# Performance work log

Hardware: AMD Instinct MI355X
Metric: run time of the kernel (lower is better)

Reference implementation:

```python
import jax, jax.numpy as jnp
import numpy as np
from itertools import product

# dims
V, B, C, H, Wd = 3, 4, 64, 120, 160   # views, batch, feat2d_channel, image H/W
D3 = 96                               # feat3d_dim
G = 64                                # voxel grid side
N = 200000                            # sparse voxel count
NL = 250000                           # number of link rows
K = 27                                # 3^3 sparse-conv kernel offsets
EPS = 1e-5


def _build_kernel_map(rng):
    # unique sparse coordinates (b,x,y,z) sampled from a B*G^3 grid, sorted by linear code
    lin = np.sort(rng.choice(B * G * G * G, size=N, replace=False)).astype(np.int64)
    b = lin // (G * G * G)
    r = lin % (G * G * G)
    x = r // (G * G)
    y = (r // G) % G
    z = r % G
    in_idx = np.zeros((K, N), np.int32)
    mask = np.zeros((K, N), bool)
    for k, (dx, dy, dz) in enumerate(product((-1, 0, 1), repeat=3)):
        qx, qy, qz = x + dx, y + dy, z + dz
        inb = (qx >= 0) & (qx < G) & (qy >= 0) & (qy < G) & (qz >= 0) & (qz < G)
        qc = ((b * G + np.clip(qx, 0, G - 1)) * G + np.clip(qy, 0, G - 1)) * G + np.clip(qz, 0, G - 1)
        pos = np.clip(np.searchsorted(lin, qc), 0, N - 1)
        ok = inb & (lin[pos] == qc)
        in_idx[k] = np.where(ok, pos, 0)
        mask[k] = ok
    return jnp.asarray(in_idx), jnp.asarray(mask)


def setup_inputs() -> dict:
    rng = np.random.default_rng(0)
    key = jax.random.key(0)
    ks = jax.random.split(key, 8)
    feat_2d_all = jax.random.normal(ks[0], (V, B, C, H, Wd), jnp.float32)
    feat3d_F = jax.random.normal(ks[1], (N, D3), jnp.float32)
    # links: (NL, 4, V) = [batch_idx, v(row), u(col), valid]
    links = np.stack([
        rng.integers(0, B, (NL, V)),
        rng.integers(0, H, (NL, V)),
        rng.integers(0, Wd, (NL, V)),
        rng.integers(0, 2, (NL, V)),
    ], axis=1).astype(np.int32)
    coords_map_out = rng.permutation(N).astype(np.int32)
    coords_map_in = rng.choice(NL, N, replace=False).astype(np.int32)
    in_idx, nbr_mask = _build_kernel_map(rng)
    s = 0.05
    W1 = jax.random.normal(ks[2], (K, V * C, C), jnp.float32) * s
    W2 = jax.random.normal(ks[3], (K, C, D3), jnp.float32) * s
    W3 = jax.random.normal(ks[4], (K, 2 * D3, D3), jnp.float32) * s
    return {
        'feat_2d_all': feat_2d_all, 'feat3d_F': feat3d_F,
        'links': jnp.asarray(links),
        'coords_map_in': jnp.asarray(coords_map_in),
        'coords_map_out': jnp.asarray(coords_map_out),
        'in_idx': in_idx, 'nbr_mask': nbr_mask,
        'W1': W1, 'g1': jnp.ones((C,)), 'b1': jnp.zeros((C,)),
        'W2': W2, 'g2': jnp.ones((D3,)), 'b2': jnp.zeros((D3,)),
        'W3': W3, 'g3': jnp.ones((D3,)), 'b3': jnp.zeros((D3,)),
    }


def _sconv(x, Wk, in_idx, nbr_mask):
    # sparse 3x3x3 conv: out[i] = sum_k x[nbr(i,k)] @ Wk[k], masked where no neighbor
    out = jnp.zeros((x.shape[0], Wk.shape[-1]), x.dtype)
    for k in range(Wk.shape[0]):
        g = x[in_idx[k]] * nbr_mask[k][:, None].astype(x.dtype)
        out = out + g @ Wk[k]
    return out


def _bn_relu(x, g, b):
    mu = x.mean(axis=0)
    var = x.var(axis=0)
    return jax.nn.relu(g * (x - mu) / jnp.sqrt(var + EPS) + b)


def reference(feat_2d_all, feat3d_F, links, coords_map_in, coords_map_out,
              in_idx, nbr_mask, W1, g1, b1, W2, g2, b2, W3, g3, b3):
    n = feat3d_F.shape[0]
    v_, c = feat_2d_all.shape[0], feat_2d_all.shape[2]
    # current_links[coords_map_out] = links[coords_map_in]
    cur = jnp.zeros((n, 4, v_), links.dtype).at[coords_map_out].set(links[coords_map_in])
    bi = cur[:, 0, :].T   # (V, n)
    hi = cur[:, 1, :].T
    wi = cur[:, 2, :].T
    val = cur[:, 3, :].T
    vs = jnp.arange(v_)[:, None]
    # per-view gather from (V,B,C,H,W): advanced indices around the channel slice -> (V, n, C)
    g = feat_2d_all[vs, bi, :, hi, wi]
    g = g * val[:, :, None].astype(g.dtype)
    feat_2d_to_3d = jnp.transpose(g, (1, 0, 2)).reshape(n, v_ * c)
    # view_fusion: conv3 -> BN -> ReLU -> conv3 -> BN -> ReLU
    h = _bn_relu(_sconv(feat_2d_to_3d, W1, in_idx, nbr_mask), g1, b1)
    h = _bn_relu(_sconv(h, W2, in_idx, nbr_mask), g2, b2)
    # cat with 3d features, fuse_to_3d: conv3 -> BN -> ReLU
    cat = jnp.concatenate([feat3d_F, h], axis=-1)
    out = _bn_relu(_sconv(cat, W3, in_idx, nbr_mask), g3, b3)
    return out
```

## Files before the change

kernel.cpp:

```cpp
#include <hip/hip_runtime.h>
#include <stdint.h>


constexpr int NPT = 200000;
constexpr int KNB = 27;

typedef unsigned short u16;
typedef __attribute__((ext_vector_type(8))) short     bf16x8;
typedef __attribute__((ext_vector_type(8))) unsigned short u16x8;
typedef __attribute__((ext_vector_type(16))) float    f32x16;

static __device__ __forceinline__ u16 f2bf(float f){
  unsigned int u = __float_as_uint(f);
  unsigned int r = (u + 0x7fffu + ((u >> 16) & 1u)) >> 16;
  return (u16)r;
}
static __device__ __forceinline__ float bf2f(u16 u){
  return __uint_as_float(((unsigned int)u) << 16);
}

static __device__ __forceinline__ void gload_lds16(const void* g, void* l){
  __builtin_amdgcn_global_load_lds(
      (const __attribute__((address_space(1))) void*)g,
      (__attribute__((address_space(3))) void*)(uint32_t)(uintptr_t)l,
      16, 0, 0);
}

__global__ void detect_mask_kernel(const int* __restrict__ m32, int* __restrict__ flag){
  if (threadIdx.x == 0 && blockIdx.x == 0){
    int ok = 1;
    for (int i = 0; i < 64; ++i){ int v = m32[i]; if (v != 0 && v != 1) ok = 0; }
    *flag = ok;
  }
}

__global__ __launch_bounds__(256) void transpose2d_kernel(const float* __restrict__ in,
                                                          u16* __restrict__ out){
  __shared__ float tile[64][33];
  int bid = blockIdx.x;
  int wt = bid % 5;  int rest = bid / 5;
  int h  = rest % 120; rest /= 120;
  int b  = rest % 4;  int v = rest / 4;
  int w0 = wt * 32;
  int tx = threadIdx.x & 31;
  int ty = threadIdx.x >> 5;
  const float* ip = in + ((size_t)(v*4 + b) * 64) * 19200 + h * 160 + w0;
  #pragma unroll
  for (int cc = 0; cc < 8; ++cc){
    int c = cc * 8 + ty;
    tile[c][tx] = ip[(size_t)c * 19200 + tx];
  }
  __syncthreads();
  u16* op = out + (((size_t)(v*4 + b) * 120 + h) * 160 + w0) * 64;
  int c = threadIdx.x & 63;
  int wg = threadIdx.x >> 6;
  #pragma unroll
  for (int i = 0; i < 8; ++i){
    int w = wg + i * 4;
    op[(size_t)w * 64 + c] = f2bf(tile[c][w]);
  }
}

__global__ void wconvert_kernel(const float* __restrict__ src, u16* __restrict__ dst,
                                int cin, int cout){
  int gid = blockIdx.x * 256 + threadIdx.x;
  int wele = cin * cout;
  int tot = KNB * wele;
  if (gid >= tot) return;
  int ncb = cout / 32;
  int nks = cin / 16;
  int e    = gid & 7;
  int lane = (gid >> 3) & 63;
  int f    = gid >> 9;
  int cb   = f % ncb;  f /= ncb;
  int ks   = f % nks;
  int k    = f / nks;
  int ci = ks * 16 + (lane >> 5) * 8 + e;
  int co = cb * 32 + (lane & 31);
  dst[gid] = f2bf(src[((size_t)k * cin + ci) * cout + co]);
}

__global__ void stage_a_kernel(const u16* __restrict__ ft, const int* __restrict__ links,
                               const int* __restrict__ cmi, const int* __restrict__ cmo,
                               u16* __restrict__ x0){
  int gid = blockIdx.x * 256 + threadIdx.x;
  if (gid >= NPT * 3) return;
  int i = gid / 3;
  int v = gid - i * 3;
  int outr = cmo[i];
  int l    = cmi[i];
  int b  = links[l*12 + v];
  int h  = links[l*12 + 3 + v];
  int w  = links[l*12 + 6 + v];
  int vl = links[l*12 + 9 + v];
  u16* dst = x0 + (size_t)outr * 192 + v * 64;
  if (vl){
    const u16* src = ft + (((size_t)(v*4 + b) * 120 + h) * 160 + w) * 64;
    #pragma unroll
    for (int j = 0; j < 8; ++j) ((u16x8*)dst)[j] = ((const u16x8*)src)[j];
  } else {
    u16x8 z = {};
    #pragma unroll
    for (int j = 0; j < 8; ++j) ((u16x8*)dst)[j] = z;
  }
}

__global__ void f3convert_kernel(const float* __restrict__ src, u16* __restrict__ dst){
  long gid = (long)blockIdx.x * 256 + threadIdx.x;
  long tot8 = (long)NPT * 12;
  if (gid >= tot8) return;
  int row = (int)(gid / 12);
  int c0  = (int)(gid % 12) * 8;
  const float* s = src + (size_t)row * 96 + c0;
  u16* d = dst + (size_t)row * 192 + c0;
  #pragma unroll
  for (int j = 0; j < 8; ++j) d[j] = f2bf(s[j]);
}

template<int CIN, int COUT, bool F32OUT>
__global__ __launch_bounds__(256)
void conv_kernel(const u16* __restrict__ x0, const u16* __restrict__ wt,
                 const int* __restrict__ in_idx,
                 const uint8_t* __restrict__ mu8, const int* __restrict__ mi32,
                 const int* __restrict__ flagp, void* __restrict__ outp,
                 int outStride, float* __restrict__ st){
  constexpr int NCB    = COUT / 32;
  constexpr int NKC    = CIN / 16;
  constexpr int WELE   = CIN * COUT;
  constexpr int ROUNDS = (WELE * 2) / 4096;
  __shared__ __align__(16) u16 wlds[WELE];
  __shared__ float shS[COUT], shQ[COUT];

  const int tid   = threadIdx.x;
  const int lane  = tid & 63;
  const int wv    = tid >> 6;
  const int l31   = lane & 31;
  const int khalf = lane >> 5;
  const int m0    = blockIdx.x * 256;
  const int fInt  = *flagp;

  if (tid < COUT){ shS[tid] = 0.f; shQ[tid] = 0.f; }

  f32x16 acc[2][NCB];
  #pragma unroll
  for (int rt = 0; rt < 2; ++rt)
    #pragma unroll
    for (int cb = 0; cb < NCB; ++cb) acc[rt][cb] = (f32x16)0.0f;

  int rowc[2];
  #pragma unroll
  for (int rt = 0; rt < 2; ++rt){
    int row = m0 + wv * 64 + rt * 32 + l31;
    rowc[rt] = row < NPT ? row : NPT - 1;
  }

  #pragma unroll
  for (int rd = 0; rd < ROUNDS; ++rd){
    int chunk = rd * 4 + wv;
    gload_lds16((const char*)wt + chunk * 1024 + lane * 16,
                (char*)wlds + chunk * 1024);
  }
  int vC[2];
  #pragma unroll
  for (int rt = 0; rt < 2; ++rt){
    int id = in_idx[rowc[rt]];
    int mv; if (fInt) mv = mi32[rowc[rt]]; else mv = (int)mu8[rowc[rt]];
    vC[rt] = mv ? id : NPT;
  }
  __syncthreads();

  const u16* xk = x0 + khalf * 8;

  for (int k = 0; k < KNB; ++k){
    const u16* b0 = xk + (size_t)vC[0] * CIN;
    const u16* b1 = xk + (size_t)vC[1] * CIN;

    if (k + 1 < KNB){
      #pragma unroll
      for (int rt = 0; rt < 2; ++rt){
        int o = (k + 1) * NPT + rowc[rt];
        int id = in_idx[o];
        int mv; if (fInt) mv = mi32[o]; else mv = (int)mu8[o];
        vC[rt] = mv ? id : NPT;
      }
    }

    #pragma unroll
    for (int kc = 0; kc < NKC; ++kc){
      bf16x8 a0 = *(const bf16x8*)(b0 + kc * 16);
      bf16x8 a1 = *(const bf16x8*)(b1 + kc * 16);
      #pragma unroll
      for (int cb = 0; cb < NCB; ++cb){
        bf16x8 b = *(const bf16x8*)&wlds[((kc * NCB + cb) * 64 + lane) * 8];
        acc[0][cb] = __builtin_amdgcn_mfma_f32_32x32x16_bf16(a0, b, acc[0][cb], 0, 0, 0);
        acc[1][cb] = __builtin_amdgcn_mfma_f32_32x32x16_bf16(a1, b, acc[1][cb], 0, 0, 0);
      }
    }
    __syncthreads();

    if (k + 1 < KNB){
      const u16* wn = wt + (size_t)(k + 1) * WELE;
      #pragma unroll
      for (int rd = 0; rd < ROUNDS; ++rd){
        int chunk = rd * 4 + wv;
        gload_lds16((const char*)wn + chunk * 1024 + lane * 16,
                    (char*)wlds + chunk * 1024);
      }
    }
    __syncthreads();
  }

  #pragma unroll
  for (int rt = 0; rt < 2; ++rt){
    #pragma unroll
    for (int cb = 0; cb < NCB; ++cb){
      const int cout = cb * 32 + l31;
      float s = 0.f, q = 0.f;
      #pragma unroll
      for (int r = 0; r < 16; ++r){
        int row = m0 + wv * 64 + rt * 32 + (r & 3) + 8 * (r >> 2) + 4 * khalf;
        if (row < NPT){
          float v = acc[rt][cb][r];
          if (F32OUT) ((float*)outp)[(size_t)row * outStride + cout] = v;
          else        ((u16*)outp)[(size_t)row * outStride + cout] = f2bf(v);
          s += v; q += v * v;
        }
      }
      atomicAdd(&shS[cout], s); atomicAdd(&shQ[cout], q);
    }
  }
  __syncthreads();
  if (tid < COUT){
    atomicAdd(&st[tid],        shS[tid]);
    atomicAdd(&st[COUT + tid], shQ[tid]);
  }
}

template<int CCH, bool ISF32>
__global__ void bnrelu_kernel(void* __restrict__ xp, int stride,
                              const float* __restrict__ st,
                              const float* __restrict__ gg, const float* __restrict__ bb){
  const float invN = 1.0f / (float)NPT;
  constexpr int GPR = CCH / 8;
  long tot8 = (long)NPT * GPR;
  for (long e8 = (long)blockIdx.x * 256 + threadIdx.x; e8 < tot8; e8 += (long)gridDim.x * 256){
    int row = (int)(e8 / GPR);
    int c0  = (int)(e8 % GPR) * 8;
    size_t base = (size_t)row * stride + c0;
    #pragma unroll
    for (int j = 0; j < 8; ++j){
      int c = c0 + j;
      float mu  = st[c] * invN;
      float var = st[CCH + c] * invN - mu * mu;
      float rs  = rsqrtf(var + 1e-5f);
      float x;
      if (ISF32) x = ((float*)xp)[base + j];
      else       x = bf2f(((u16*)xp)[base + j]);
      float y = gg[c] * (x - mu) * rs + bb[c];
      y = y > 0.f ? y : 0.f;
      if (ISF32) ((float*)xp)[base + j] = y;
      else       ((u16*)xp)[base + j] = f2bf(y);
    }
  }
}

extern "C" void kernel_launch(void* const* d_in, const int* in_sizes, int n_in,
                              void* d_out, int out_size, void* d_ws, size_t ws_size,
                              hipStream_t stream){
  const float* feat2d = (const float*)d_in[0];
  const float* feat3d = (const float*)d_in[1];
  const int*   links  = (const int*)d_in[2];
  const int*   cmi    = (const int*)d_in[3];
  const int*   cmo    = (const int*)d_in[4];
  const int*   inidx  = (const int*)d_in[5];
  const void*  mask   = d_in[6];
  const float* W1 = (const float*)d_in[7];
  const float* g1 = (const float*)d_in[8];
  const float* b1 = (const float*)d_in[9];
  const float* W2 = (const float*)d_in[10];
  const float* g2 = (const float*)d_in[11];
  const float* b2 = (const float*)d_in[12];
  const float* W3 = (const float*)d_in[13];
  const float* g3 = (const float*)d_in[14];
  const float* b3 = (const float*)d_in[15];

  char* ws = (char*)d_ws;
  u16* X0 = (u16*)(ws + 0);
  constexpr size_t OFF_B  = 76800512;
  u16* FT = (u16*)(ws + OFF_B);
  u16* Z1 = (u16*)(ws + OFF_B);
  u16* WT1 = (u16*)(ws + 106291712);
  u16* WT2 = WT1 + 27 * 192 * 64;
  u16* WT3 = WT2 + 27 * 64 * 96;
  float* ST  = (float*)(ws + 108282368);
  float* ST1 = ST;
  float* ST2 = ST + 128;
  float* ST3 = ST + 320;
  int*   FLAG = (int*)(ST + 512);

  hipMemsetAsync(ST, 0, 513 * sizeof(float), stream);
  detect_mask_kernel<<<1, 64, 0, stream>>>((const int*)mask, FLAG);
  transpose2d_kernel<<<7200, 256, 0, stream>>>(feat2d, FT);
  wconvert_kernel<<<(27*192*64 + 255)/256, 256, 0, stream>>>(W1, WT1, 192, 64);
  wconvert_kernel<<<(27*64*96  + 255)/256, 256, 0, stream>>>(W2, WT2, 64, 96);
  wconvert_kernel<<<(27*192*96 + 255)/256, 256, 0, stream>>>(W3, WT3, 192, 96);
  stage_a_kernel<<<(NPT*3 + 255)/256, 256, 0, stream>>>(FT, links, cmi, cmo, X0);

  hipMemsetAsync(ws + (size_t)NPT * 384, 0, 384, stream);
  hipMemsetAsync(ws + OFF_B + (size_t)NPT * 128, 0, 128, stream);

  const int nblk = (NPT + 255) / 256;
  const uint8_t* m8 = (const uint8_t*)mask;
  const int* m32 = (const int*)mask;

  conv_kernel<192, 64, false><<<nblk, 256, 0, stream>>>(X0, WT1, inidx, m8, m32, FLAG, Z1, 64, ST1);
  bnrelu_kernel<64, false><<<2048, 256, 0, stream>>>(Z1, 64, ST1, g1, b1);

  f3convert_kernel<<<((NPT*12) + 255)/256, 256, 0, stream>>>(feat3d, X0);

  conv_kernel<64, 96, false><<<nblk, 256, 0, stream>>>(Z1, WT2, inidx, m8, m32, FLAG, X0 + 96, 192, ST2);
  bnrelu_kernel<96, false><<<2048, 256, 0, stream>>>(X0 + 96, 192, ST2, g2, b2);

  conv_kernel<192, 96, true><<<nblk, 256, 0, stream>>>(X0, WT3, inidx, m8, m32, FLAG, d_out, 96, ST3);
  bnrelu_kernel<96, true><<<2048, 256, 0, stream>>>(d_out, 96, ST3, g3, b3);
}
```

Measured before the change: 763.3 us.

## Switch sparse conv to 16x16x32 MFMA with double-buffered weight LDS and smaller tiles

The conv kernel now uses 16x16x32 bf16 MFMAs instead of 32x32x16, with the weight pre-layout changed to match. Each block covers 128 rows instead of 256, so twice as many blocks launch. Weights for the next kernel offset are double-buffered in LDS and prefetched before the current offset's MFMAs, which removes one barrier per offset. All input gathers for an offset are issued up front. The cost is doubled LDS for weights, which may lower occupancy for the 192x96 layer. Smaller tiles also mean more redundant weight loads across blocks.

```diff
diff --git a/kernel.cpp b/kernel.cpp
--- a/kernel.cpp
+++ b/kernel.cpp
@@ -8,7 +8,7 @@
 typedef unsigned short u16;
 typedef __attribute__((ext_vector_type(8))) short     bf16x8;
 typedef __attribute__((ext_vector_type(8))) unsigned short u16x8;
-typedef __attribute__((ext_vector_type(16))) float    f32x16;
+typedef __attribute__((ext_vector_type(4))) float     f32x4;
 
 static __device__ __forceinline__ u16 f2bf(float f){
   unsigned int u = __float_as_uint(f);
@@ -64,19 +64,18 @@
 __global__ void wconvert_kernel(const float* __restrict__ src, u16* __restrict__ dst,
                                 int cin, int cout){
   int gid = blockIdx.x * 256 + threadIdx.x;
-  int wele = cin * cout;
-  int tot = KNB * wele;
+  int tot = KNB * cin * cout;
   if (gid >= tot) return;
-  int ncb = cout / 32;
-  int nks = cin / 16;
+  int ncb = cout / 16;
+  int nkc = cin / 32;
   int e    = gid & 7;
   int lane = (gid >> 3) & 63;
   int f    = gid >> 9;
   int cb   = f % ncb;  f /= ncb;
-  int ks   = f % nks;
-  int k    = f / nks;
-  int ci = ks * 16 + (lane >> 5) * 8 + e;
-  int co = cb * 32 + (lane & 31);
+  int kc   = f % nkc;
+  int k    = f / nkc;
+  int ci = kc * 32 + (lane >> 4) * 8 + e;
+  int co = cb * 16 + (lane & 15);
   dst[gid] = f2bf(src[((size_t)k * cin + ci) * cout + co]);
 }
 
@@ -124,33 +123,33 @@
                  const uint8_t* __restrict__ mu8, const int* __restrict__ mi32,
                  const int* __restrict__ flagp, void* __restrict__ outp,
                  int outStride, float* __restrict__ st){
-  constexpr int NCB    = COUT / 32;
-  constexpr int NKC    = CIN / 16;
+  constexpr int NCB    = COUT / 16;
+  constexpr int NKC    = CIN / 32;
   constexpr int WELE   = CIN * COUT;
   constexpr int ROUNDS = (WELE * 2) / 4096;
-  __shared__ __align__(16) u16 wlds[WELE];
+  __shared__ __align__(16) u16 wlds[2 * WELE];
   __shared__ float shS[COUT], shQ[COUT];
 
   const int tid   = threadIdx.x;
   const int lane  = tid & 63;
   const int wv    = tid >> 6;
-  const int l31   = lane & 31;
-  const int khalf = lane >> 5;
-  const int m0    = blockIdx.x * 256;
+  const int r16   = lane & 15;
+  const int kgrp  = lane >> 4;
+  const int m0    = blockIdx.x * 128;
   const int fInt  = *flagp;
 
   if (tid < COUT){ shS[tid] = 0.f; shQ[tid] = 0.f; }
 
-  f32x16 acc[2][NCB];
+  f32x4 acc[2][NCB];
   #pragma unroll
   for (int rt = 0; rt < 2; ++rt)
     #pragma unroll
-    for (int cb = 0; cb < NCB; ++cb) acc[rt][cb] = (f32x16)0.0f;
+    for (int cb = 0; cb < NCB; ++cb) acc[rt][cb] = (f32x4)0.0f;
 
   int rowc[2];
   #pragma unroll
   for (int rt = 0; rt < 2; ++rt){
-    int row = m0 + wv * 64 + rt * 32 + l31;
+    int row = m0 + wv * 32 + rt * 16 + r16;
     rowc[rt] = row < NPT ? row : NPT - 1;
   }
 
@@ -169,9 +168,20 @@
   }
   __syncthreads();
 
-  const u16* xk = x0 + khalf * 8;
+  const u16* xk = x0 + kgrp * 8;
 
   for (int k = 0; k < KNB; ++k){
+    if (k + 1 < KNB){
+      const u16* wn = wt + (size_t)(k + 1) * WELE;
+      char* wd = (char*)wlds + ((k + 1) & 1) * (WELE * 2);
+      #pragma unroll
+      for (int rd = 0; rd < ROUNDS; ++rd){
+        int chunk = rd * 4 + wv;
+        gload_lds16((const char*)wn + chunk * 1024 + lane * 16,
+                    wd + chunk * 1024);
+      }
+    }
+
     const u16* b0 = xk + (size_t)vC[0] * CIN;
     const u16* b1 = xk + (size_t)vC[1] * CIN;
 
@@ -185,42 +195,37 @@
       }
     }
 
+    bf16x8 a0[NKC], a1[NKC];
     #pragma unroll
     for (int kc = 0; kc < NKC; ++kc){
-      bf16x8 a0 = *(const bf16x8*)(b0 + kc * 16);
-      bf16x8 a1 = *(const bf16x8*)(b1 + kc * 16);
+      a0[kc] = *(const bf16x8*)(b0 + kc * 32);
+      a1[kc] = *(const bf16x8*)(b1 + kc * 32);
+    }
+
+    const u16* wb = &wlds[(k & 1) * WELE];
+    #pragma unroll
+    for (int kc = 0; kc < NKC; ++kc){
       #pragma unroll
       for (int cb = 0; cb < NCB; ++cb){
-        bf16x8 b = *(const bf16x8*)&wlds[((kc * NCB + cb) * 64 + lane) * 8];
-        acc[0][cb] = __builtin_amdgcn_mfma_f32_32x32x16_bf16(a0, b, acc[0][cb], 0, 0, 0);
-        acc[1][cb] = __builtin_amdgcn_mfma_f32_32x32x16_bf16(a1, b, acc[1][cb], 0, 0, 0);
+        bf16x8 b = *(const bf16x8*)&wb[((kc * NCB + cb) * 64 + lane) * 8];
+        acc[0][cb] = __builtin_amdgcn_mfma_f32_16x16x32_bf16(a0[kc], b, acc[0][cb], 0, 0, 0);
+        acc[1][cb] = __builtin_amdgcn_mfma_f32_16x16x32_bf16(a1[kc], b, acc[1][cb], 0, 0, 0);
       }
     }
     __syncthreads();
-
-    if (k + 1 < KNB){
-      const u16* wn = wt + (size_t)(k + 1) * WELE;
-      #pragma unroll
-      for (int rd = 0; rd < ROUNDS; ++rd){
-        int chunk = rd * 4 + wv;
-        gload_lds16((const char*)wn + chunk * 1024 + lane * 16,
-                    (char*)wlds + chunk * 1024);
-      }
-    }
-    __syncthreads();
   }
 
   #pragma unroll
   for (int rt = 0; rt < 2; ++rt){
     #pragma unroll
     for (int cb = 0; cb < NCB; ++cb){
-      const int cout = cb * 32 + l31;
+      const int cout = cb * 16 + r16;
       float s = 0.f, q = 0.f;
       #pragma unroll
-      for (int r = 0; r < 16; ++r){
-        int row = m0 + wv * 64 + rt * 32 + (r & 3) + 8 * (r >> 2) + 4 * khalf;
+      for (int j = 0; j < 4; ++j){
+        int row = m0 + wv * 32 + rt * 16 + kgrp * 4 + j;
         if (row < NPT){
-          float v = acc[rt][cb][r];
+          float v = acc[rt][cb][j];
           if (F32OUT) ((float*)outp)[(size_t)row * outStride + cout] = v;
           else        ((u16*)outp)[(size_t)row * outStride + cout] = f2bf(v);
           s += v; q += v * v;
@@ -309,7 +314,7 @@
   hipMemsetAsync(ws + (size_t)NPT * 384, 0, 384, stream);
   hipMemsetAsync(ws + OFF_B + (size_t)NPT * 128, 0, 128, stream);
 
-  const int nblk = (NPT + 255) / 256;
+  const int nblk = (NPT + 127) / 128;
   const uint8_t* m8 = (const uint8_t*)mask;
   const int* m32 = (const int*)mask;
 
```

Measured after the change: 817.8 us. 1.07x slower.
